# Optimization experiments

Hardware: AMD Instinct MI355X
Metric: run time of the kernel (lower is better)

The kernel has to match this reference:

```python
import jax, jax.numpy as jnp
import numpy as np
from jax import lax

N_NODES = 1_000_000
N_EDGES = 4_000_000
N_GRAPHS = 25_000
XT_LEN = 735
DIM = 32
BN_EPS = 1e-5


def setup_inputs() -> dict:
    key = jax.random.key(0)
    ks = jax.random.split(key, 32)

    def lin(k, i, o):
        return (jax.random.normal(k, (i, o), jnp.float32) / np.float32(np.sqrt(i)))

    inp = {}
    inp["x"] = jax.random.normal(ks[0], (N_NODES, 78), jnp.float32)
    inp["edge_index"] = jax.random.randint(ks[1], (2, N_EDGES), 0, N_NODES)
    inp["batch"] = jnp.sort(jax.random.randint(ks[2], (N_NODES,), 0, N_GRAPHS))
    inp["xo"] = jax.random.normal(ks[3], (N_GRAPHS, 1, XT_LEN), jnp.float32)

    # GIN layer 1 MLP: 78 -> 32 -> 32
    inp["gin1_W1"] = lin(ks[4], 78, DIM); inp["gin1_b1"] = jnp.zeros((DIM,), jnp.float32)
    inp["gin1_W2"] = lin(ks[5], DIM, DIM); inp["gin1_b2"] = jnp.zeros((DIM,), jnp.float32)
    # GIN layers 2..5 MLPs: 32 -> 32 -> 32 (stacked)
    inp["gins_W1"] = jax.random.normal(ks[6], (4, DIM, DIM), jnp.float32) / np.float32(np.sqrt(DIM))
    inp["gins_b1"] = jnp.zeros((4, DIM), jnp.float32)
    inp["gins_W2"] = jax.random.normal(ks[7], (4, DIM, DIM), jnp.float32) / np.float32(np.sqrt(DIM))
    inp["gins_b2"] = jnp.zeros((4, DIM), jnp.float32)
    # BatchNorm params for all 5 layers
    inp["bn_gamma"] = jnp.ones((5, DIM), jnp.float32)
    inp["bn_beta"] = jnp.zeros((5, DIM), jnp.float32)
    # drug head
    inp["fc1_xd_W"] = lin(ks[8], DIM, 128); inp["fc1_xd_b"] = jnp.zeros((128,), jnp.float32)
    # omics CNN
    inp["cnn1_W"] = jax.random.normal(ks[9], (32, 1, 8), jnp.float32) / np.float32(np.sqrt(8))
    inp["cnn1_b"] = jnp.zeros((32,), jnp.float32)
    inp["cnn2_W"] = jax.random.normal(ks[10], (64, 32, 8), jnp.float32) / np.float32(np.sqrt(32 * 8))
    inp["cnn2_b"] = jnp.zeros((64,), jnp.float32)
    inp["cnn3_W"] = jax.random.normal(ks[11], (128, 64, 8), jnp.float32) / np.float32(np.sqrt(64 * 8))
    inp["cnn3_b"] = jnp.zeros((128,), jnp.float32)
    inp["fc1_xt_W"] = lin(ks[12], 2944, 128); inp["fc1_xt_b"] = jnp.zeros((128,), jnp.float32)
    # combined head
    inp["fc1_W"] = lin(ks[13], 256, 1024); inp["fc1_b"] = jnp.zeros((1024,), jnp.float32)
    inp["fc2_W"] = lin(ks[14], 1024, 128); inp["fc2_b"] = jnp.zeros((128,), jnp.float32)
    inp["out_W"] = lin(ks[15], 128, 1); inp["out_b"] = jnp.zeros((1,), jnp.float32)
    return inp


def _gin_layer(h, edge_index, W1, b1, W2, b2, gamma, beta):
    # GINConv (eps=0): MLP(x + sum_{j in N(i)} x_j), then ReLU then BatchNorm1d.
    agg = jax.ops.segment_sum(h[edge_index[0]], edge_index[1], num_segments=h.shape[0])
    z = h + agg
    z = jax.nn.relu(z @ W1 + b1) @ W2 + b2
    z = jax.nn.relu(z)
    # BatchNorm1d with batch statistics (training-mode normalization)
    mu = z.mean(axis=0)
    var = z.var(axis=0)
    return gamma * (z - mu) / jnp.sqrt(var + BN_EPS) + beta


def _conv1d(x, W, b):
    y = lax.conv_general_dilated(x, W, (1,), 'VALID', dimension_numbers=('NCH', 'OIH', 'NCH'))
    return y + b[None, :, None]


def _maxpool3(x):
    return lax.reduce_window(x, -jnp.inf, lax.max, (1, 1, 3), (1, 1, 3), 'VALID')


def reference(x, edge_index, batch, xo,
              gin1_W1, gin1_b1, gin1_W2, gin1_b2,
              gins_W1, gins_b1, gins_W2, gins_b2,
              bn_gamma, bn_beta,
              fc1_xd_W, fc1_xd_b,
              cnn1_W, cnn1_b, cnn2_W, cnn2_b, cnn3_W, cnn3_b,
              fc1_xt_W, fc1_xt_b,
              fc1_W, fc1_b, fc2_W, fc2_b, out_W, out_b):
    B = xo.shape[0]
    # drug GNN branch: 5 GIN layers
    h = _gin_layer(x, edge_index, gin1_W1, gin1_b1, gin1_W2, gin1_b2, bn_gamma[0], bn_beta[0])
    for i in range(4):
        h = _gin_layer(h, edge_index, gins_W1[i], gins_b1[i], gins_W2[i], gins_b2[i],
                       bn_gamma[i + 1], bn_beta[i + 1])
    pooled = jax.ops.segment_sum(h, batch, num_segments=B)   # global_add_pool -> [B, 32]
    xd = jax.nn.relu(pooled @ fc1_xd_W + fc1_xd_b)            # dropout inactive (eval)

    # omics CNN branch
    t = _maxpool3(jax.nn.relu(_conv1d(xo, cnn1_W, cnn1_b)))
    t = _maxpool3(jax.nn.relu(_conv1d(t, cnn2_W, cnn2_b)))
    t = _maxpool3(jax.nn.relu(_conv1d(t, cnn3_W, cnn3_b)))
    xt = t.reshape(B, -1) @ fc1_xt_W + fc1_xt_b               # [B, 128]

    # combined head
    xc = jnp.concatenate([xd, xt], axis=1)                    # [B, 256]
    xc = jax.nn.relu(xc @ fc1_W + fc1_b)
    xc = jax.nn.relu(xc @ fc2_W + fc2_b)
    return xc @ out_W + out_b                                 # [B, 1]
```

## Files before the change

kernel.cpp:

```cpp
#include <hip/hip_runtime.h>

#define NN 1000000
#define NE 4000000
#define NG 25000
#define BN_EPS 1e-5f

typedef unsigned short u16t;
typedef unsigned int u32t;
typedef __attribute__((ext_vector_type(8))) short bf16x8;
typedef __attribute__((ext_vector_type(8))) _Float16 f16x8;
typedef __attribute__((ext_vector_type(4))) float f32x4;

__device__ inline u16t f2bf(float f) {
  u32t u = __float_as_uint(f);
  u32t r = (u + 0x7FFFu + ((u >> 16) & 1u)) >> 16;
  return (u16t)r;
}
__device__ inline float bf2f(u16t h) { return __uint_as_float((u32t)h << 16); }
__device__ inline u16t f2h(float f) {
  _Float16 h = (_Float16)f;
  return *(u16t*)&h;
}
__device__ inline float h2f(u16t v) {
  _Float16 h = *(_Float16*)&v;
  return (float)h;
}
__device__ inline void add8h(float* a, uint4 v) {
  union { uint4 u; _Float16 h[8]; } cv;
  cv.u = v;
#pragma unroll
  for (int j = 0; j < 8; ++j) a[j] += (float)cv.h[j];
}

static const size_t OFF_U    = 0;
static const size_t OFF_T3   = 0;
static const size_t OFF_YA   = 150000000;
static const size_t OFF_YB   = 214000000;
static const size_t OFF_ST   = 278000000;
static const size_t OFF_RS   = 279000000;
static const size_t OFF_CUR  = 283200000;
static const size_t OFF_BSUM = 287300000;
static const size_t OFF_SSRC = 288000000;
static const size_t OFF_WK   = 304000000;
static const size_t OFF_XC   = 306000000;
static const size_t OFF_H1   = 150000000;
static const size_t OFF_H2   = 214000000;

__global__ __launch_bounds__(256) void k_hist(const int* __restrict__ ei, u32t* __restrict__ cnt) {
  const int i = blockIdx.x * 256 + threadIdx.x;
  if (i < NE) atomicAdd(&cnt[ei[NE + i]], 1u);
}

__global__ __launch_bounds__(256) void k_scan1(const u32t* __restrict__ deg, u32t* __restrict__ bsum) {
  __shared__ u32t red[4];
  const int b = blockIdx.x, t = threadIdx.x;
  u32t s = 0;
#pragma unroll
  for (int j = 0; j < 4; ++j) {
    const int i = b * 1024 + j * 256 + t;
    if (i < NN) s += deg[i];
  }
#pragma unroll
  for (int off = 32; off > 0; off >>= 1) s += __shfl_down(s, off);
  if ((t & 63) == 0) red[t >> 6] = s;
  __syncthreads();
  if (t == 0) bsum[b] = red[0] + red[1] + red[2] + red[3];
}

__global__ __launch_bounds__(256) void k_scan2(u32t* __restrict__ bsum, u32t* __restrict__ rs, int nblk) {
  __shared__ u32t sh[256];
  const int t = threadIdx.x;
  u32t v[4];
#pragma unroll
  for (int j = 0; j < 4; ++j) {
    const int i = t * 4 + j;
    v[j] = (i < nblk) ? bsum[i] : 0u;
  }
  const u32t tot = v[0] + v[1] + v[2] + v[3];
  sh[t] = tot;
  __syncthreads();
  for (int off = 1; off < 256; off <<= 1) {
    u32t add = (t >= off) ? sh[t - off] : 0u;
    __syncthreads();
    sh[t] += add;
    __syncthreads();
  }
  const u32t tb = (t == 0) ? 0u : sh[t - 1];
  u32t run = tb;
#pragma unroll
  for (int j = 0; j < 4; ++j) {
    const int i = t * 4 + j;
    if (i < nblk) bsum[i] = run;
    run += v[j];
  }
  if (t == 0) rs[NN] = NE;
}

__global__ __launch_bounds__(256) void k_scan3(u32t* __restrict__ cur, u32t* __restrict__ rs,
                                               const u32t* __restrict__ bsum) {
  __shared__ u32t sh[256];
  const int b = blockIdx.x, t = threadIdx.x;
  const int i0 = b * 1024 + t * 4;
  u32t v[4];
#pragma unroll
  for (int j = 0; j < 4; ++j) v[j] = (i0 + j < NN) ? cur[i0 + j] : 0u;
  sh[t] = v[0] + v[1] + v[2] + v[3];
  __syncthreads();
  for (int off = 1; off < 256; off <<= 1) {
    u32t add = (t >= off) ? sh[t - off] : 0u;
    __syncthreads();
    sh[t] += add;
    __syncthreads();
  }
  u32t run = bsum[b] + ((t == 0) ? 0u : sh[t - 1]);
#pragma unroll
  for (int j = 0; j < 4; ++j) {
    const int i = i0 + j;
    if (i < NN) { rs[i] = run; cur[i] = run; }
    run += v[j];
  }
}

__global__ __launch_bounds__(256) void k_scatter(const int* __restrict__ ei,
                                                 u32t* __restrict__ cur, int* __restrict__ ssrc,
                                                 int pass) {
  const int i = blockIdx.x * 256 + threadIdx.x;
  if (i < NE) {
    const int dst = ei[NE + i];
    if ((dst >> 17) == pass) {
      const int src = ei[i];
      const u32t pos = atomicAdd(&cur[dst], 1u);
      ssrc[pos] = src;
    }
  }
}


__global__ __launch_bounds__(256) void k_mlp1_first(
    const float* __restrict__ x, const float* __restrict__ W1, u16t* __restrict__ u)
{
  __shared__ __align__(16) u16t Xh[64 * 104];
  __shared__ __align__(16) u16t Wt[32 * 104];
  __shared__ __align__(16) u16t Uh[64 * 40];
  const int t = threadIdx.x;
  const int n0b = blockIdx.x * 64;
  for (int id = t; id < 64 * 78; id += 256) {
    const int row = id / 78, k = id - row * 78;
    Xh[row * 104 + k] = f2h(x[(size_t)n0b * 78 + id]);
  }
  for (int id = t; id < 64 * 18; id += 256) {
    const int row = id / 18, k = 78 + (id - row * 18);
    Xh[row * 104 + k] = 0;
  }
  for (int id = t; id < 78 * 32; id += 256) {
    const int k = id >> 5, c = id & 31;
    Wt[c * 104 + k] = f2h(W1[id]);
  }
  for (int id = t; id < 32 * 18; id += 256) {
    const int c = id / 18, k = 78 + (id - c * 18);
    Wt[c * 104 + k] = 0;
  }
  __syncthreads();
  {
    const int w = t >> 6, l = t & 63, col = l & 15, kg = l >> 4;
    const int m0 = w * 16;
    f32x4 ac0 = {0.f, 0.f, 0.f, 0.f}, ac1 = {0.f, 0.f, 0.f, 0.f};
#pragma unroll
    for (int ks = 0; ks < 3; ++ks) {
      const f16x8 af = *(const f16x8*)(Xh + (m0 + col) * 104 + ks * 32 + kg * 8);
      const f16x8 bf0 = *(const f16x8*)(Wt + col * 104 + ks * 32 + kg * 8);
      const f16x8 bf1 = *(const f16x8*)(Wt + (16 + col) * 104 + ks * 32 + kg * 8);
      ac0 = __builtin_amdgcn_mfma_f32_16x16x32_f16(af, bf0, ac0, 0, 0, 0);
      ac1 = __builtin_amdgcn_mfma_f32_16x16x32_f16(af, bf1, ac1, 0, 0, 0);
    }
#pragma unroll
    for (int r = 0; r < 4; ++r) {
      const int m = m0 + kg * 4 + r;
      Uh[m * 40 + col] = f2h(ac0[r]);
      Uh[m * 40 + 16 + col] = f2h(ac1[r]);
    }
  }
  __syncthreads();
  {
    const int row = t >> 2;
    const uint4 v = *(const uint4*)(Uh + row * 40 + (t & 3) * 8);
    *(uint4*)(u + (size_t)(n0b + row) * 32 + (t & 3) * 8) = v;
  }
}

__global__ __launch_bounds__(256) void k_agg0(
    const u16t* __restrict__ u, const u32t* __restrict__ rs, const int* __restrict__ ssrc,
    const float* __restrict__ b1, const float* __restrict__ W2, const float* __restrict__ b2,
    u16t* __restrict__ yout, float* __restrict__ stats_out)
{
  __shared__ __align__(16) u16t W2t[32 * 40];
  __shared__ __align__(16) u16t A1h[64 * 40];
  __shared__ __align__(16) u16t A2h[64 * 40];
  __shared__ float red[256];
  __shared__ u32t rss[65];
  const int t = threadIdx.x;
  const int n0b = blockIdx.x * 64;
  for (int id = t; id < 1024; id += 256) {
    int k = id >> 5, c = id & 31;
    W2t[c * 40 + k] = f2h(W2[id]);
  }
  if (t < 65) rss[t] = rs[n0b + t];
  __syncthreads();
  const int nl = t >> 2, c0 = (t & 3) * 8;
  {
    const int n = n0b + nl;
    float a[8] = {};
    add8h(a, *(const uint4*)(u + (size_t)n * 32 + c0));
    const u32t e0 = rss[nl], e1 = rss[nl + 1];
    u32t e = e0;
    for (; e + 4 <= e1; e += 4) {
      const int s0v = ssrc[e], s1v = ssrc[e + 1], s2v = ssrc[e + 2], s3v = ssrc[e + 3];
      const uint4 v0 = *(const uint4*)(u + (size_t)s0v * 32 + c0);
      const uint4 v1 = *(const uint4*)(u + (size_t)s1v * 32 + c0);
      const uint4 v2 = *(const uint4*)(u + (size_t)s2v * 32 + c0);
      const uint4 v3 = *(const uint4*)(u + (size_t)s3v * 32 + c0);
      add8h(a, v0); add8h(a, v1); add8h(a, v2); add8h(a, v3);
    }
    for (; e < e1; ++e)
      add8h(a, *(const uint4*)(u + (size_t)ssrc[e] * 32 + c0));
    union { u16t h[8]; uint4 v; } pk;
#pragma unroll
    for (int j = 0; j < 8; ++j) pk.h[j] = f2h(fmaxf(a[j] + b1[c0 + j], 0.f));
    *(uint4*)(A1h + nl * 40 + c0) = pk.v;
  }
  __syncthreads();
  {
    const int w = t >> 6, l = t & 63, col = l & 15, kg = l >> 4;
    const int m0 = w * 16;
    const f16x8 af = *(const f16x8*)(A1h + (m0 + col) * 40 + kg * 8);
    const f16x8 bf0 = *(const f16x8*)(W2t + col * 40 + kg * 8);
    const f16x8 bf1 = *(const f16x8*)(W2t + (16 + col) * 40 + kg * 8);
    f32x4 ac0 = {0.f, 0.f, 0.f, 0.f}, ac1 = {0.f, 0.f, 0.f, 0.f};
    ac0 = __builtin_amdgcn_mfma_f32_16x16x32_f16(af, bf0, ac0, 0, 0, 0);
    ac1 = __builtin_amdgcn_mfma_f32_16x16x32_f16(af, bf1, ac1, 0, 0, 0);
    const float bb0 = b2[col], bb1 = b2[16 + col];
#pragma unroll
    for (int r = 0; r < 4; ++r) {
      const int m = m0 + kg * 4 + r;
      A2h[m * 40 + col] = f2h(fmaxf(ac0[r] + bb0, 0.f));
      A2h[m * 40 + 16 + col] = f2h(fmaxf(ac1[r] + bb1, 0.f));
    }
  }
  __syncthreads();
  const int c = t & 31;
  float rsum = 0.f, rq = 0.f;
#pragma unroll
  for (int rep = 0; rep < 8; ++rep) {
    const int row = (t >> 5) + rep * 8;
    const float v = h2f(A2h[row * 40 + c]);
    rsum += v;
    rq += v * v;
  }
  {
    const int row = t >> 2;
    const uint4 v = *(const uint4*)(A2h + row * 40 + (t & 3) * 8);
    *(uint4*)(yout + (size_t)(n0b + row) * 32 + (t & 3) * 8) = v;
  }
  rsum += __shfl_down(rsum, 32);
  rq += __shfl_down(rq, 32);
  __syncthreads();
  const int wv_ = t >> 6, lane = t & 63;
  if (lane < 32) {
    red[wv_ * 32 + lane] = rsum;
    red[128 + wv_ * 32 + lane] = rq;
  }
  __syncthreads();
  if (t < 32) {
    float aa = red[t] + red[32 + t] + red[64 + t] + red[96 + t];
    float bb = red[128 + t] + red[160 + t] + red[192 + t] + red[224 + t];
    unsafeAtomicAdd(&stats_out[t], aa);
    unsafeAtomicAdd(&stats_out[32 + t], bb);
  }
}

__device__ __forceinline__ void layer_body(
    int bid, char* smem,
    const u16t* __restrict__ yin, const u32t* __restrict__ rs, const int* __restrict__ ssrc,
    const float* __restrict__ stats, const float* __restrict__ gamma, const float* __restrict__ beta,
    const float* __restrict__ W1, const float* __restrict__ b1,
    const float* __restrict__ W2, const float* __restrict__ b2,
    u16t* __restrict__ yout, float* __restrict__ stats_out)
{
  u16t* W1t = (u16t*)smem;
  u16t* W2t = (u16t*)(smem + 2560);
  u16t* A1h = (u16t*)(smem + 5120);
  u16t* A2h = (u16t*)(smem + 10240);
  float* red = (float*)(smem + 15360);
  u32t* rss = (u32t*)(smem + 16384);
  const int t = threadIdx.x;
  const int n0b = bid * 64;
  for (int id = t; id < 1024; id += 256) {
    int k = id >> 5, c = id & 31;
    W1t[c * 40 + k] = f2h(W1[id]);
    W2t[c * 40 + k] = f2h(W2[id]);
  }
  if (t < 65) rss[t] = rs[n0b + t];
  __syncthreads();
  const int nl = t >> 2, c0 = (t & 3) * 8;
  {
    const int n = n0b + nl;
    float sc[8], sh[8];
#pragma unroll
    for (int j = 0; j < 8; ++j) {
      const int c = c0 + j;
      const float mu = stats[c] * (1.f / NN);
      float var = fmaxf(stats[32 + c] * (1.f / NN) - mu * mu, 0.f);
      sc[j] = gamma[c] * rsqrtf(var + BN_EPS);
      sh[j] = beta[c] - mu * sc[j];
    }
    float a[8] = {};
    add8h(a, *(const uint4*)(yin + (size_t)n * 32 + c0));
    const u32t e0 = rss[nl], e1 = rss[nl + 1];
    u32t e = e0;
    for (; e + 4 <= e1; e += 4) {
      const int s0v = ssrc[e], s1v = ssrc[e + 1], s2v = ssrc[e + 2], s3v = ssrc[e + 3];
      const uint4 v0 = *(const uint4*)(yin + (size_t)s0v * 32 + c0);
      const uint4 v1 = *(const uint4*)(yin + (size_t)s1v * 32 + c0);
      const uint4 v2 = *(const uint4*)(yin + (size_t)s2v * 32 + c0);
      const uint4 v3 = *(const uint4*)(yin + (size_t)s3v * 32 + c0);
      add8h(a, v0); add8h(a, v1); add8h(a, v2); add8h(a, v3);
    }
    for (; e < e1; ++e)
      add8h(a, *(const uint4*)(yin + (size_t)ssrc[e] * 32 + c0));
    const float cnt = (float)(e1 - e0 + 1u);
    union { u16t h[8]; uint4 v; } pk;
#pragma unroll
    for (int j = 0; j < 8; ++j) pk.h[j] = f2h(sc[j] * a[j] + cnt * sh[j]);
    *(uint4*)(A1h + nl * 40 + c0) = pk.v;
  }
  __syncthreads();
  const int w = t >> 6, l = t & 63, col = l & 15, kg = l >> 4;
  const int m0 = w * 16;
  {
    const f16x8 af = *(const f16x8*)(A1h + (m0 + col) * 40 + kg * 8);
    const f16x8 bf0 = *(const f16x8*)(W1t + col * 40 + kg * 8);
    const f16x8 bf1 = *(const f16x8*)(W1t + (16 + col) * 40 + kg * 8);
    f32x4 ac0 = {0.f, 0.f, 0.f, 0.f}, ac1 = {0.f, 0.f, 0.f, 0.f};
    ac0 = __builtin_amdgcn_mfma_f32_16x16x32_f16(af, bf0, ac0, 0, 0, 0);
    ac1 = __builtin_amdgcn_mfma_f32_16x16x32_f16(af, bf1, ac1, 0, 0, 0);
    const float bb0 = b1[col], bb1 = b1[16 + col];
#pragma unroll
    for (int r = 0; r < 4; ++r) {
      const int m = m0 + kg * 4 + r;
      A2h[m * 40 + col] = f2h(fmaxf(ac0[r] + bb0, 0.f));
      A2h[m * 40 + 16 + col] = f2h(fmaxf(ac1[r] + bb1, 0.f));
    }
  }
  __syncthreads();
  {
    const f16x8 af = *(const f16x8*)(A2h + (m0 + col) * 40 + kg * 8);
    const f16x8 bf0 = *(const f16x8*)(W2t + col * 40 + kg * 8);
    const f16x8 bf1 = *(const f16x8*)(W2t + (16 + col) * 40 + kg * 8);
    f32x4 ac0 = {0.f, 0.f, 0.f, 0.f}, ac1 = {0.f, 0.f, 0.f, 0.f};
    ac0 = __builtin_amdgcn_mfma_f32_16x16x32_f16(af, bf0, ac0, 0, 0, 0);
    ac1 = __builtin_amdgcn_mfma_f32_16x16x32_f16(af, bf1, ac1, 0, 0, 0);
    const float bb0 = b2[col], bb1 = b2[16 + col];
#pragma unroll
    for (int r = 0; r < 4; ++r) {
      const int m = m0 + kg * 4 + r;
      A1h[m * 40 + col] = f2h(fmaxf(ac0[r] + bb0, 0.f));
      A1h[m * 40 + 16 + col] = f2h(fmaxf(ac1[r] + bb1, 0.f));
    }
  }
  __syncthreads();
  const int c = t & 31;
  float rsum = 0.f, rq = 0.f;
#pragma unroll
  for (int rep = 0; rep < 8; ++rep) {
    const int row = (t >> 5) + rep * 8;
    const float v = h2f(A1h[row * 40 + c]);
    rsum += v;
    rq += v * v;
  }
  {
    const int row = t >> 2;
    const uint4 v = *(const uint4*)(A1h + row * 40 + (t & 3) * 8);
    *(uint4*)(yout + (size_t)(n0b + row) * 32 + (t & 3) * 8) = v;
  }
  rsum += __shfl_down(rsum, 32);
  rq += __shfl_down(rq, 32);
  __syncthreads();
  const int wv_ = t >> 6, lane = t & 63;
  if (lane < 32) {
    red[wv_ * 32 + lane] = rsum;
    red[128 + wv_ * 32 + lane] = rq;
  }
  __syncthreads();
  if (t < 32) {
    float aa = red[t] + red[32 + t] + red[64 + t] + red[96 + t];
    float bb = red[128 + t] + red[160 + t] + red[192 + t] + red[224 + t];
    unsafeAtomicAdd(&stats_out[t], aa);
    unsafeAtomicAdd(&stats_out[32 + t], bb);
  }
}

__device__ __forceinline__ void cnn_body(
    int g, char* smem,
    const float* __restrict__ xo,
    const float* __restrict__ w1, const float* __restrict__ b1,
    const u16t* __restrict__ W2k, const float* __restrict__ b2,
    const u16t* __restrict__ W3k, const float* __restrict__ b3,
    u16t* __restrict__ t3)
{
  float* xot = (float*)(smem);
  float* w1s = (float*)(smem + 3072);
  float* b2s = (float*)(smem + 4096);
  float* b3s = (float*)(smem + 4352);
  short* T1T = (short*)(smem + 4864);
  char*  T2B = smem + 20736;
  u16t*  stg = (u16t*)(smem + 4864);

  const int t = threadIdx.x;
  const int w = t >> 6, l = t & 63, col = l & 15, kg = l >> 4;

  for (int i = t; i < 768; i += 256) xot[i] = (i < 735) ? xo[(size_t)g * 735 + i] : 0.f;
  w1s[t] = w1[t];
  if (t < 64) b2s[t] = b2[t];
  if (t < 128) b3s[t] = b3[t];
  if (t < 192) {
    int r = 242 + (t >> 5), c = t & 31;
    T1T[r * 32 + c] = 0;
  }
  __syncthreads();

  {
    const int c = t >> 3, qg = t & 7;
    float wv[8];
#pragma unroll
    for (int j = 0; j < 8; ++j) wv[j] = w1s[c * 8 + j];
    const float bias = b1[c];
    const int q0 = qg * 31, qe = (q0 + 31 < 242) ? q0 + 31 : 242;
#pragma unroll 1
    for (int qc = q0; qc < qe; qc += 10) {
      const int cnt = (qe - qc < 10) ? qe - qc : 10;
      float xv[37];
#pragma unroll
      for (int j = 0; j < 37; ++j) xv[j] = xot[3 * qc + j];
#pragma unroll
      for (int j0 = 0; j0 < 10; ++j0) {
        if (j0 < cnt) {
          float a0 = bias, a1 = bias, a2 = bias;
#pragma unroll
          for (int tt = 0; tt < 8; ++tt) {
            a0 = fmaf(wv[tt], xv[3 * j0 + tt], a0);
            a1 = fmaf(wv[tt], xv[3 * j0 + 1 + tt], a1);
            a2 = fmaf(wv[tt], xv[3 * j0 + 2 + tt], a2);
          }
          float m = fmaxf(fmaxf(a0, a1), fmaxf(a2, 0.f));
          const int pos = qc + j0;
          T1T[pos * 32 + (c ^ ((pos & 3) << 3))] = (short)f2bf(m);
        }
      }
    }
  }
  __syncthreads();

  {
    bf16x8 am[8];
#pragma unroll
    for (int kk = 0; kk < 8; ++kk)
      am[kk] = *(const bf16x8*)(W2k + (w * 16 + col) * 256 + kk * 32 + kg * 8);
#pragma unroll 1
    for (int qt = 0; qt < 5; ++qt) {
      const int rbase = qt * 48 + col * 3;
      bf16x8 rv[10];
#pragma unroll
      for (int s = 0; s < 10; ++s) {
        const int row = rbase + s;
        rv[s] = *(const bf16x8*)(T1T + row * 32 + ((kg ^ (row & 3)) << 3));
      }
      f32x4 a0 = {0.f, 0.f, 0.f, 0.f}, a1 = a0, a2 = a0;
#pragma unroll
      for (int kk = 0; kk < 8; ++kk) {
        a0 = __builtin_amdgcn_mfma_f32_16x16x32_bf16(am[kk], rv[kk], a0, 0, 0, 0);
        a1 = __builtin_amdgcn_mfma_f32_16x16x32_bf16(am[kk], rv[kk + 1], a1, 0, 0, 0);
        a2 = __builtin_amdgcn_mfma_f32_16x16x32_bf16(am[kk], rv[kk + 2], a2, 0, 0, 0);
      }
      const int q = qt * 16 + col;
      if (q < 78) {
        union { u16t u[4]; uint2 v; } pk;
#pragma unroll
        for (int r = 0; r < 4; ++r) {
          const float bb = b2s[w * 16 + kg * 4 + r];
          float m = fmaxf(fmaxf(a0[r], a1[r]), a2[r]);
          pk.u[r] = f2bf(fmaxf(m + bb, 0.f));
        }
        const int boff = (q * 128 + (w * 16 + kg * 4) * 2) ^ ((q & 7) << 4);
        *(uint2*)(T2B + boff) = pk.v;
      }
    }
  }
  __syncthreads();

  {
#pragma unroll 1
    for (int mi = 0; mi < 2; ++mi) {
      const int m3 = w * 2 + mi;
      f32x4 acc[2][3];
#pragma unroll
      for (int qt = 0; qt < 2; ++qt)
#pragma unroll
        for (int r = 0; r < 3; ++r) acc[qt][r] = (f32x4){0.f, 0.f, 0.f, 0.f};
#pragma unroll 1
      for (int kh = 0; kh < 2; ++kh) {
        bf16x8 amh[8];
#pragma unroll
        for (int tt = 0; tt < 8; ++tt)
          amh[tt] = *(const bf16x8*)(W3k + (m3 * 16 + col) * 512 + (tt * 2 + kh) * 32 + kg * 8);
#pragma unroll
        for (int qt = 0; qt < 2; ++qt) {
          const int rbase = qt * 48 + col * 3;
          bf16x8 rv[10];
#pragma unroll
          for (int s = 0; s < 10; ++s) {
            int row = rbase + s;
            row = (row < 78) ? row : 77;
            const int boff = (row * 128 + kh * 64 + kg * 16) ^ ((row & 7) << 4);
            rv[s] = *(const bf16x8*)(T2B + boff);
          }
#pragma unroll
          for (int tt = 0; tt < 8; ++tt) {
            acc[qt][0] = __builtin_amdgcn_mfma_f32_16x16x32_bf16(amh[tt], rv[tt], acc[qt][0], 0, 0, 0);
            acc[qt][1] = __builtin_amdgcn_mfma_f32_16x16x32_bf16(amh[tt], rv[tt + 1], acc[qt][1], 0, 0, 0);
            acc[qt][2] = __builtin_amdgcn_mfma_f32_16x16x32_bf16(amh[tt], rv[tt + 2], acc[qt][2], 0, 0, 0);
          }
        }
      }
#pragma unroll
      for (int qt = 0; qt < 2; ++qt) {
        const int q = qt * 16 + col;
        if (q < 23) {
#pragma unroll
          for (int r = 0; r < 4; ++r) {
            const int c = m3 * 16 + kg * 4 + r;
            float m = fmaxf(fmaxf(acc[qt][0][r], acc[qt][1][r]), acc[qt][2][r]);
            stg[c * 23 + q] = f2bf(fmaxf(m + b3s[c], 0.f));
          }
        }
      }
    }
  }
  __syncthreads();

  {
    const uint4* s4 = (const uint4*)stg;
    uint4* d4 = (uint4*)(t3 + (size_t)g * 2944);
    for (int id = t; id < 368; id += 256) d4[id] = s4[id];
  }
}

__global__ __launch_bounds__(256, 4) void k_fused(
    const u16t* __restrict__ yin, const u32t* __restrict__ rs, const int* __restrict__ ssrc,
    const float* __restrict__ stats, const float* __restrict__ gamma, const float* __restrict__ beta,
    const float* __restrict__ W1, const float* __restrict__ b1,
    const float* __restrict__ W2, const float* __restrict__ b2,
    u16t* __restrict__ yout, float* __restrict__ stats_out,
    const float* __restrict__ xo, const float* __restrict__ c1W, const float* __restrict__ c1b,
    const u16t* __restrict__ W2k, const float* __restrict__ c2b,
    const u16t* __restrict__ W3k, const float* __restrict__ c3b,
    u16t* __restrict__ t3, int cnn_g0)
{
  __shared__ __align__(16) char smem[30720];
  const int grp = blockIdx.x / 7, rem = blockIdx.x % 7;
  if (rem < 5)
    layer_body(grp * 5 + rem, smem, yin, rs, ssrc, stats, gamma, beta,
               W1, b1, W2, b2, yout, stats_out);
  else
    cnn_body(cnn_g0 + grp * 2 + (rem - 5), smem, xo, c1W, c1b, W2k, c2b, W3k, c3b, t3);
}

__global__ __launch_bounds__(64) void k_pool_xd(
    const u16t* __restrict__ y, const int* __restrict__ batch,
    const float* __restrict__ stats, const float* __restrict__ gamma,
    const float* __restrict__ beta, const float* __restrict__ Wxd,
    const float* __restrict__ bxd, u16t* __restrict__ xc)
{
  const int g = blockIdx.x, t = threadIdx.x;
  int lo = 0, n = NN;
  while (n > 0) {
    int h = n >> 1, m = lo + h;
    if (batch[m] < g) { lo = m + 1; n -= h + 1; } else n = h;
  }
  int hi = lo;
  n = NN - lo;
  while (n > 0) {
    int h = n >> 1, m = hi + h;
    if (batch[m] < g + 1) { hi = m + 1; n -= h + 1; } else n = h;
  }
  const int c = t & 31;
  const float mu = stats[4 * 64 + c] * (1.f / NN);
  float var = fmaxf(stats[4 * 64 + 32 + c] * (1.f / NN) - mu * mu, 0.f);
  const float sc = gamma[4 * 32 + c] * rsqrtf(var + BN_EPS);
  const float sh = beta[4 * 32 + c] - mu * sc;
  float acc = 0.f;
  for (int i = lo + (t >> 5); i < hi; i += 2) acc += h2f(y[(size_t)i * 32 + c]);
  acc += __shfl_down(acc, 32);
  __shared__ float pl[32];
  if (t < 32) pl[t] = acc * sc + (float)(hi - lo) * sh;
  __syncthreads();
#pragma unroll
  for (int rep = 0; rep < 2; ++rep) {
    const int o = t + rep * 64;
    float a = bxd[o];
#pragma unroll
    for (int cc = 0; cc < 32; ++cc) a = fmaf(pl[cc], Wxd[cc * 128 + o], a);
    xc[(size_t)g * 256 + o] = f2bf(fmaxf(a, 0.f));
  }
}

__global__ __launch_bounds__(256) void k_prep(
    const float* __restrict__ w2, const float* __restrict__ w3,
    const float* __restrict__ wxt, const float* __restrict__ wf1, const float* __restrict__ wf2,
    u16t* __restrict__ W2k, u16t* __restrict__ W3k,
    u16t* __restrict__ WXT, u16t* __restrict__ WF1, u16t* __restrict__ WF2)
{
  const int i = blockIdx.x * 256 + threadIdx.x;
  if (i < 64 * 256) {
    int c2 = i >> 8, kk = i & 255, tt = kk >> 5, ci = kk & 31;
    W2k[i] = f2bf(w2[c2 * 256 + ci * 8 + tt]);
  }
  if (i < 128 * 512) {
    int c3 = i >> 9, kk = i & 511, tt = kk >> 6, ci = kk & 63;
    W3k[i] = f2bf(w3[c3 * 512 + ci * 8 + tt]);
  }
  if (i < 128 * 2944) {
    int nn = i / 2944, kk = i - nn * 2944;
    WXT[i] = f2bf(wxt[kk * 128 + nn]);
  }
  if (i < 1024 * 256) {
    int nn = i >> 8, kk = i & 255;
    WF1[i] = f2bf(wf1[kk * 1024 + nn]);
  }
  if (i < 128 * 1024) {
    int nn = i >> 10, kk = i & 1023;
    WF2[i] = f2bf(wf2[kk * 128 + nn]);
  }
}

__global__ __launch_bounds__(256) void k_mgemm(
    const u16t* __restrict__ A, int lda,
    const u16t* __restrict__ WT, const float* __restrict__ bias,
    void* __restrict__ Cv, int ldc, int c_off, int M, int Kd,
    int relu_f, int out32)
{
  __shared__ __align__(16) u16t As[128 * 4 * 8];
  __shared__ __align__(16) u16t Ws2[64 * 4 * 8];
  const int t = threadIdx.x;
  const int w = t >> 6, l = t & 63, col = l & 15, kg = l >> 4;
  const int wm = w & 1, wn = w >> 1;
  const int m0 = blockIdx.x * 128, n0 = blockIdx.y * 64;
  f32x4 acc[4][2];
#pragma unroll
  for (int i = 0; i < 4; ++i)
#pragma unroll
    for (int j = 0; j < 2; ++j) acc[i][j] = (f32x4){0.f, 0.f, 0.f, 0.f};
  const int ar = t >> 1, ac = (t & 1) * 2;
  const int wr = t >> 2, wc = t & 3;
  const bool aok = (m0 + ar) < M;
  const u16t* Ap = A + (size_t)(m0 + ar) * lda;
  const u16t* Wp = WT + (size_t)(n0 + wr) * Kd;
  for (int k0 = 0; k0 < Kd; k0 += 32) {
    bf16x8 av0 = {0, 0, 0, 0, 0, 0, 0, 0}, av1 = {0, 0, 0, 0, 0, 0, 0, 0};
    if (aok) {
      av0 = *(const bf16x8*)(Ap + k0 + ac * 8);
      av1 = *(const bf16x8*)(Ap + k0 + (ac + 1) * 8);
    }
    const bf16x8 wv = *(const bf16x8*)(Wp + k0 + wc * 8);
    __syncthreads();
    *(bf16x8*)(As + (ar * 4 + (ac ^ (ar & 3))) * 8) = av0;
    *(bf16x8*)(As + (ar * 4 + ((ac + 1) ^ (ar & 3))) * 8) = av1;
    *(bf16x8*)(Ws2 + (wr * 4 + (wc ^ (wr & 3))) * 8) = wv;
    __syncthreads();
    bf16x8 af[4], bf[2];
#pragma unroll
    for (int i = 0; i < 4; ++i) {
      const int R = wm * 64 + i * 16 + col;
      af[i] = *(const bf16x8*)(As + (R * 4 + (kg ^ (R & 3))) * 8);
    }
#pragma unroll
    for (int j = 0; j < 2; ++j) {
      const int R = wn * 32 + j * 16 + col;
      bf[j] = *(const bf16x8*)(Ws2 + (R * 4 + (kg ^ (R & 3))) * 8);
    }
#pragma unroll
    for (int i = 0; i < 4; ++i)
#pragma unroll
      for (int j = 0; j < 2; ++j)
        acc[i][j] = __builtin_amdgcn_mfma_f32_16x16x32_bf16(af[i], bf[j], acc[i][j], 0, 0, 0);
  }
#pragma unroll
  for (int j = 0; j < 2; ++j) {
    const int gn = n0 + wn * 32 + j * 16 + col;
    const float bb = bias[gn];
#pragma unroll
    for (int i = 0; i < 4; ++i) {
      const int gmb = m0 + wm * 64 + i * 16 + kg * 4;
#pragma unroll
      for (int r = 0; r < 4; ++r) {
        const int gm = gmb + r;
        if (gm < M) {
          float v = acc[i][j][r] + bb;
          if (relu_f) v = fmaxf(v, 0.f);
          if (out32) ((float*)Cv)[(size_t)gm * ldc + c_off + gn] = v;
          else ((u16t*)Cv)[(size_t)gm * ldc + c_off + gn] = f2bf(v);
        }
      }
    }
  }
}

__global__ __launch_bounds__(256) void k_out(
    const float* __restrict__ h2, const float* __restrict__ Wo,
    const float* __restrict__ bo, float* __restrict__ out)
{
  __shared__ float Ws_[128];
  const int t = threadIdx.x;
  if (t < 128) Ws_[t] = Wo[t];
  __syncthreads();
  const int g = blockIdx.x * 32 + (t >> 3), l = t & 7;
  float acc = 0.f;
  if (g < NG) {
    const float* hr = h2 + (size_t)g * 128 + l * 16;
    const float* wr = Ws_ + l * 16;
#pragma unroll
    for (int j = 0; j < 16; ++j) acc = fmaf(hr[j], wr[j], acc);
  }
  acc += __shfl_down(acc, 4, 8);
  acc += __shfl_down(acc, 2, 8);
  acc += __shfl_down(acc, 1, 8);
  if (l == 0 && g < NG) out[g] = acc + bo[0];
}

extern "C" void kernel_launch(void* const* d_in, const int* in_sizes, int n_in,
                              void* d_out, int out_size, void* d_ws, size_t ws_size,
                              hipStream_t stream) {
  const float* x    = (const float*)d_in[0];
  const int*   ei   = (const int*)d_in[1];
  const int*   batch= (const int*)d_in[2];
  const float* xo   = (const float*)d_in[3];
  const float* g1W1 = (const float*)d_in[4];
  const float* g1b1 = (const float*)d_in[5];
  const float* g1W2 = (const float*)d_in[6];
  const float* g1b2 = (const float*)d_in[7];
  const float* gsW1 = (const float*)d_in[8];
  const float* gsb1 = (const float*)d_in[9];
  const float* gsW2 = (const float*)d_in[10];
  const float* gsb2 = (const float*)d_in[11];
  const float* bng  = (const float*)d_in[12];
  const float* bnb  = (const float*)d_in[13];
  const float* Wxd  = (const float*)d_in[14];
  const float* bxd  = (const float*)d_in[15];
  const float* c1W  = (const float*)d_in[16];
  const float* c1b  = (const float*)d_in[17];
  const float* c2W  = (const float*)d_in[18];
  const float* c2b  = (const float*)d_in[19];
  const float* c3W  = (const float*)d_in[20];
  const float* c3b  = (const float*)d_in[21];
  const float* Wxt  = (const float*)d_in[22];
  const float* bxt  = (const float*)d_in[23];
  const float* W1f  = (const float*)d_in[24];
  const float* b1f  = (const float*)d_in[25];
  const float* W2f  = (const float*)d_in[26];
  const float* b2f  = (const float*)d_in[27];
  const float* Wo   = (const float*)d_in[28];
  const float* bo   = (const float*)d_in[29];

  char* ws = (char*)d_ws;
  u16t*  U    = (u16t*)(ws + OFF_U);
  u16t*  YA   = (u16t*)(ws + OFF_YA);
  u16t*  YB   = (u16t*)(ws + OFF_YB);
  float* ST   = (float*)(ws + OFF_ST);
  u32t*  RS   = (u32t*)(ws + OFF_RS);
  u32t*  CUR  = (u32t*)(ws + OFF_CUR);
  u32t*  BS   = (u32t*)(ws + OFF_BSUM);
  int*   SSRC = (int*)(ws + OFF_SSRC);
  u16t*  WK   = (u16t*)(ws + OFF_WK);
  u16t*  W2K  = WK;
  u16t*  W3K  = WK + 16384;
  u16t*  WXT  = WK + 16384 + 65536;
  u16t*  WF1  = WK + 16384 + 65536 + 376832;
  u16t*  WF2  = WK + 16384 + 65536 + 376832 + 262144;
  u16t*  XC   = (u16t*)(ws + OFF_XC);
  u16t*  T3   = (u16t*)(ws + OFF_T3);
  u16t*  H1   = (u16t*)(ws + OFF_H1);
  float* H2   = (float*)(ws + OFF_H2);
  float* OUT  = (float*)d_out;

  const int NBLK = (NN + 1023) / 1024;

  hipMemsetAsync(ST, 0, 5 * 64 * sizeof(float), stream);
  hipMemsetAsync(CUR, 0, NN * sizeof(u32t), stream);

  k_prep<<<(128 * 2944 + 255) / 256, 256, 0, stream>>>(c2W, c3W, Wxt, W1f, W2f,
                                                        W2K, W3K, WXT, WF1, WF2);

  k_hist<<<(NE + 255) / 256, 256, 0, stream>>>(ei, CUR);
  k_scan1<<<NBLK, 256, 0, stream>>>(CUR, BS);
  k_scan2<<<1, 256, 0, stream>>>(BS, RS, NBLK);
  k_scan3<<<NBLK, 256, 0, stream>>>(CUR, RS, BS);
  for (int p = 0; p < 8; ++p)
    k_scatter<<<(NE + 255) / 256, 256, 0, stream>>>(ei, CUR, SSRC, p);

  k_mlp1_first<<<NN / 64, 256, 0, stream>>>(x, g1W1, U);
  k_agg0<<<NN / 64, 256, 0, stream>>>(U, RS, SSRC, g1b1, g1W2, g1b2, YA, ST + 0);

  const u16t* yin = YA;
  u16t* yout = YB;
  for (int lyr = 1; lyr <= 4; ++lyr) {
    k_fused<<<21875, 256, 0, stream>>>(yin, RS, SSRC, ST + (lyr - 1) * 64,
                                       bng + (lyr - 1) * 32, bnb + (lyr - 1) * 32,
                                       gsW1 + (lyr - 1) * 1024, gsb1 + (lyr - 1) * 32,
                                       gsW2 + (lyr - 1) * 1024, gsb2 + (lyr - 1) * 32,
                                       yout, ST + lyr * 64,
                                       xo, c1W, c1b, W2K, c2b, W3K, c3b, T3,
                                       (lyr - 1) * 6250);
    const u16t* tmp = yin;
    yin = yout;
    yout = (u16t*)tmp;
  }
  k_pool_xd<<<NG, 64, 0, stream>>>(yin, batch, ST, bng, bnb, Wxd, bxd, XC);

  {
    dim3 grid((NG + 127) / 128, 2);
    k_mgemm<<<grid, 256, 0, stream>>>(T3, 2944, WXT, bxt, XC, 256, 128, NG, 2944, 0, 0);
  }
  {
    dim3 grid((NG + 127) / 128, 16);
    k_mgemm<<<grid, 256, 0, stream>>>(XC, 256, WF1, b1f, H1, 1024, 0, NG, 256, 1, 0);
  }
  {
    dim3 grid((NG + 127) / 128, 2);
    k_mgemm<<<grid, 256, 0, stream>>>(H1, 1024, WF2, b2f, H2, 128, 0, NG, 1024, 1, 1);
  }
  k_out<<<(NG + 31) / 32, 256, 0, stream>>>(H2, Wo, bo, OUT);
}
```

Before: 1.999 ms.

## Spread omics CNN work across all five GIN aggregation launches

```diff
diff --git a/kernel.cpp b/kernel.cpp
--- a/kernel.cpp
+++ b/kernel.cpp
@@ -32,7 +32,6 @@
   for (int j = 0; j < 8; ++j) a[j] += (float)cv.h[j];
 }
 
-static const size_t OFF_U    = 0;
 static const size_t OFF_T3   = 0;
 static const size_t OFF_YA   = 150000000;
 static const size_t OFF_YB   = 214000000;
@@ -43,6 +42,7 @@
 static const size_t OFF_SSRC = 288000000;
 static const size_t OFF_WK   = 304000000;
 static const size_t OFF_XC   = 306000000;
+static const size_t OFF_U    = 320000000;
 static const size_t OFF_H1   = 150000000;
 static const size_t OFF_H2   = 214000000;
 
@@ -188,18 +188,19 @@
   }
 }
 
-__global__ __launch_bounds__(256) void k_agg0(
+__device__ __forceinline__ void agg0_body(
+    int bid, char* smem,
     const u16t* __restrict__ u, const u32t* __restrict__ rs, const int* __restrict__ ssrc,
     const float* __restrict__ b1, const float* __restrict__ W2, const float* __restrict__ b2,
     u16t* __restrict__ yout, float* __restrict__ stats_out)
 {
-  __shared__ __align__(16) u16t W2t[32 * 40];
-  __shared__ __align__(16) u16t A1h[64 * 40];
-  __shared__ __align__(16) u16t A2h[64 * 40];
-  __shared__ float red[256];
-  __shared__ u32t rss[65];
+  u16t* W2t = (u16t*)(smem + 2560);
+  u16t* A1h = (u16t*)(smem + 5120);
+  u16t* A2h = (u16t*)(smem + 10240);
+  float* red = (float*)(smem + 15360);
+  u32t* rss = (u32t*)(smem + 16384);
   const int t = threadIdx.x;
-  const int n0b = blockIdx.x * 64;
+  const int n0b = bid * 64;
   for (int id = t; id < 1024; id += 256) {
     int k = id >> 5, c = id & 31;
     W2t[c * 40 + k] = f2h(W2[id]);
@@ -554,6 +555,23 @@
   }
 }
 
+__global__ __launch_bounds__(256, 4) void k_fused0(
+    const u16t* __restrict__ u, const u32t* __restrict__ rs, const int* __restrict__ ssrc,
+    const float* __restrict__ b1, const float* __restrict__ W2, const float* __restrict__ b2,
+    u16t* __restrict__ yout, float* __restrict__ stats_out,
+    const float* __restrict__ xo, const float* __restrict__ c1W, const float* __restrict__ c1b,
+    const u16t* __restrict__ W2k, const float* __restrict__ c2b,
+    const u16t* __restrict__ W3k, const float* __restrict__ c3b,
+    u16t* __restrict__ t3, int cnn_g0)
+{
+  __shared__ __align__(16) char smem[30720];
+  const int grp = blockIdx.x / 33, rem = blockIdx.x % 33;
+  if (rem < 25)
+    agg0_body(grp * 25 + rem, smem, u, rs, ssrc, b1, W2, b2, yout, stats_out);
+  else
+    cnn_body(cnn_g0 + grp * 8 + (rem - 25), smem, xo, c1W, c1b, W2k, c2b, W3k, c3b, t3);
+}
+
 __global__ __launch_bounds__(256, 4) void k_fused(
     const u16t* __restrict__ yin, const u32t* __restrict__ rs, const int* __restrict__ ssrc,
     const float* __restrict__ stats, const float* __restrict__ gamma, const float* __restrict__ beta,
@@ -566,12 +584,12 @@
     u16t* __restrict__ t3, int cnn_g0)
 {
   __shared__ __align__(16) char smem[30720];
-  const int grp = blockIdx.x / 7, rem = blockIdx.x % 7;
-  if (rem < 5)
-    layer_body(grp * 5 + rem, smem, yin, rs, ssrc, stats, gamma, beta,
+  const int grp = blockIdx.x / 33, rem = blockIdx.x % 33;
+  if (rem < 25)
+    layer_body(grp * 25 + rem, smem, yin, rs, ssrc, stats, gamma, beta,
                W1, b1, W2, b2, yout, stats_out);
   else
-    cnn_body(cnn_g0 + grp * 2 + (rem - 5), smem, xo, c1W, c1b, W2k, c2b, W3k, c3b, t3);
+    cnn_body(cnn_g0 + grp * 8 + (rem - 25), smem, xo, c1W, c1b, W2k, c2b, W3k, c3b, t3);
 }
 
 __global__ __launch_bounds__(64) void k_pool_xd(
@@ -807,18 +825,20 @@
     k_scatter<<<(NE + 255) / 256, 256, 0, stream>>>(ei, CUR, SSRC, p);
 
   k_mlp1_first<<<NN / 64, 256, 0, stream>>>(x, g1W1, U);
-  k_agg0<<<NN / 64, 256, 0, stream>>>(U, RS, SSRC, g1b1, g1W2, g1b2, YA, ST + 0);
+
+  k_fused0<<<20625, 256, 0, stream>>>(U, RS, SSRC, g1b1, g1W2, g1b2, YA, ST + 0,
+                                      xo, c1W, c1b, W2K, c2b, W3K, c3b, T3, 0);
 
   const u16t* yin = YA;
   u16t* yout = YB;
   for (int lyr = 1; lyr <= 4; ++lyr) {
-    k_fused<<<21875, 256, 0, stream>>>(yin, RS, SSRC, ST + (lyr - 1) * 64,
+    k_fused<<<20625, 256, 0, stream>>>(yin, RS, SSRC, ST + (lyr - 1) * 64,
                                        bng + (lyr - 1) * 32, bnb + (lyr - 1) * 32,
                                        gsW1 + (lyr - 1) * 1024, gsb1 + (lyr - 1) * 32,
                                        gsW2 + (lyr - 1) * 1024, gsb2 + (lyr - 1) * 32,
                                        yout, ST + lyr * 64,
                                        xo, c1W, c1b, W2K, c2b, W3K, c3b, T3,
-                                       (lyr - 1) * 6250);
+                                       lyr * 5000);
     const u16t* tmp = yin;
     yin = yout;
     yout = (u16t*)tmp;
```

New measurement: 1.953 ms. -2.3%, faster.
